# Optimization experiments

Measured on AMD Instinct MI355X. Metric: run time of the kernel, lower is better.

## Reference

```python
import jax, jax.numpy as jnp
import numpy as np

NUM_SLOTS = 8
SLOT_DIM = 256
ITERS = 3
EPS = 1e-8
SCALE = SLOT_DIM ** -0.5


def _ln(x, g, b, eps=1e-5):
    m = jnp.mean(x, axis=-1, keepdims=True)
    v = jnp.mean(jnp.square(x - m), axis=-1, keepdims=True)
    return (x - m) * jax.lax.rsqrt(v + eps) * g + b


def setup_inputs() -> dict:
    key = jax.random.key(0)
    ks = jax.random.split(key, 16)
    b, n, c = 32, 1024, 256
    d = SLOT_DIM
    def xavier(k, shape):
        fan_in, fan_out = shape[1], shape[0]
        lim = np.sqrt(6.0 / (fan_in + fan_out))
        return jax.random.uniform(k, shape, jnp.float32, -lim, lim)
    lim_mu = np.sqrt(6.0 / (1 + d))
    return {
        "inputs": jax.random.normal(ks[0], (b, n, c), jnp.float32),
        "noise": jax.random.normal(ks[1], (b, NUM_SLOTS, d), jnp.float32),
        "slots_mu": jax.random.uniform(ks[2], (1, 1, d), jnp.float32, -lim_mu, lim_mu),
        "slots_log_sigma": jax.random.uniform(ks[3], (1, 1, d), jnp.float32, -lim_mu, lim_mu),
        "Wq": xavier(ks[4], (d, d)),
        "Wk": xavier(ks[5], (d, c)),
        "Wv": xavier(ks[6], (d, c)),
        "gru_wih": xavier(ks[7], (3 * d, d)),
        "gru_whh": xavier(ks[8], (3 * d, d)),
        "gru_bih": jnp.zeros((3 * d,), jnp.float32),
        "gru_bhh": jnp.zeros((3 * d,), jnp.float32),
        "mlp_w1": xavier(ks[9], (4 * d, d)),
        "mlp_b1": jnp.zeros((4 * d,), jnp.float32),
        "mlp_w2": xavier(ks[10], (d, 4 * d)),
        "mlp_b2": jnp.zeros((d,), jnp.float32),
        "ln_in_g": jnp.ones((c,), jnp.float32),
        "ln_in_b": jnp.zeros((c,), jnp.float32),
        "ln_s_g": jnp.ones((d,), jnp.float32),
        "ln_s_b": jnp.zeros((d,), jnp.float32),
        "ln_ff_g": jnp.ones((d,), jnp.float32),
        "ln_ff_b": jnp.zeros((d,), jnp.float32),
    }


def reference(inputs, noise, slots_mu, slots_log_sigma, Wq, Wk, Wv,
              gru_wih, gru_whh, gru_bih, gru_bhh,
              mlp_w1, mlp_b1, mlp_w2, mlp_b2,
              ln_in_g, ln_in_b, ln_s_g, ln_s_b, ln_ff_g, ln_ff_b):
    b = inputs.shape[0]
    d = SLOT_DIM
    # slots ~ N(mu, sigma) reparameterized with given noise
    slots = slots_mu + jnp.exp(slots_log_sigma) * noise  # [b, S, d]
    x = _ln(inputs, ln_in_g, ln_in_b)
    k = jnp.einsum('bnc,dc->bnd', x, Wk)
    v = jnp.einsum('bnc,dc->bnd', x, Wv)
    for _ in range(ITERS):
        slots_prev = slots
        s = _ln(slots, ln_s_g, ln_s_b)
        q = jnp.einsum('bid,ed->bie', s, Wq)
        dots = jnp.einsum('bid,bjd->bij', q, k) * SCALE  # [b, S, n]
        attn = jax.nn.softmax(dots, axis=1) + EPS         # softmax over slots
        attn = attn / jnp.sum(attn, axis=-1, keepdims=True)
        updates = jnp.einsum('bjd,bij->bid', v, attn)      # [b, S, d]
        # GRUCell: x=updates, h=slots_prev (flattened over batch*slots)
        u = updates.reshape(-1, d)
        h = slots_prev.reshape(-1, d)
        gi = u @ gru_wih.T + gru_bih
        gh = h @ gru_whh.T + gru_bhh
        i_r, i_z, i_n = jnp.split(gi, 3, axis=-1)
        h_r, h_z, h_n = jnp.split(gh, 3, axis=-1)
        r = jax.nn.sigmoid(i_r + h_r)
        z = jax.nn.sigmoid(i_z + h_z)
        nn_ = jnp.tanh(i_n + r * h_n)
        slots = ((1.0 - z) * nn_ + z * h).reshape(b, -1, d)
        ff = _ln(slots, ln_ff_g, ln_ff_b)
        ff = jax.nn.relu(ff @ mlp_w1.T + mlp_b1) @ mlp_w2.T + mlp_b2
        slots = slots + ff
    return slots
```

## Files before the change

kernel.cpp:

```cpp
#include <hip/hip_runtime.h>


typedef __attribute__((ext_vector_type(8))) __bf16 bf16x8;
typedef __attribute__((ext_vector_type(4))) float  f32x4;

#define MFMA16(a, b, c) __builtin_amdgcn_mfma_f32_16x16x32_bf16((a), (b), (c), 0, 0, 0)

static __device__ __forceinline__ unsigned short f2bf(float f) {
    unsigned int x = __float_as_uint(f);
    x = (x + 0x7fffu + ((x >> 16) & 1u)) >> 16;
    return (unsigned short)x;
}
static __device__ __forceinline__ float bf2f(unsigned short u) {
    return __uint_as_float((unsigned int)u << 16);
}
static __device__ __forceinline__ float bflo(unsigned int x) {
    return __uint_as_float(x << 16);
}
static __device__ __forceinline__ float bfhi(unsigned int x) {
    return __uint_as_float(x & 0xffff0000u);
}

struct Params {
    const float *inputs, *noise, *mu, *ls;
    const float *Wq, *Wk, *Wv, *wih, *whh, *bih, *bhh, *w1, *b1, *w2, *b2;
    const float *ln_in_g, *ln_in_b, *ln_s_g, *ln_s_b, *ln_ff_g, *ln_ff_b;
    float* out;
    unsigned short *x_bf, *kvW_bf, *Wq_bf, *wih_bf, *whh_bf, *w1_bf, *w2_bf;
    unsigned short *kv_bf, *h_bf, *ff_bf, *h1_bf;
    float *slots, *q, *upart, *rspart, *gi, *gh, *opart;
};

static __device__ void qgemm(const Params& p, const unsigned short (&u)[16][264], int r0) {
    const int t = threadIdx.x, w = t >> 6, lane = t & 63;
    const int lr = lane & 15, lq = lane >> 4;
    f32x4 acc[4] = {};
    for (int k0 = 0; k0 < 256; k0 += 32) {
        bf16x8 a = *(const bf16x8*)&u[lr][k0 + lq * 8];
        #pragma unroll
        for (int j = 0; j < 4; ++j) {
            bf16x8 bv = *(const bf16x8*)(p.Wq_bf + (size_t)(w * 64 + j * 16 + lr) * 256 + k0 + lq * 8);
            acc[j] = MFMA16(a, bv, acc[j]);
        }
    }
    #pragma unroll
    for (int j = 0; j < 4; ++j)
        #pragma unroll
        for (int r = 0; r < 4; ++r)
            p.q[(size_t)(r0 + lq * 4 + r) * 256 + w * 64 + j * 16 + lr] = acc[j][r];
}

__global__ __launch_bounds__(256) void k_prep(Params p) {
    const int bid = blockIdx.x, t = threadIdx.x;
    for (int gid = bid * 256 + t; gid < 1179648; gid += 4608 * 256) {
        if      (gid <   65536) p.kvW_bf[gid]          = f2bf(p.Wk[gid]);
        else if (gid <  131072) p.kvW_bf[gid]          = f2bf(p.Wv[gid -   65536]);
        else if (gid <  196608) p.Wq_bf[gid - 131072]  = f2bf(p.Wq[gid -  131072]);
        else if (gid <  393216) p.wih_bf[gid - 196608] = f2bf(p.wih[gid - 196608]);
        else if (gid <  589824) p.whh_bf[gid - 393216] = f2bf(p.whh[gid - 393216]);
        else if (gid <  851968) p.w1_bf[gid - 589824]  = f2bf(p.w1[gid -  589824]);
        else if (gid < 1114112) p.w2_bf[gid - 851968]  = f2bf(p.w2[gid -  851968]);
        else {
            const int i = gid - 1114112;
            const int d = i & 255;
            p.slots[i] = p.mu[d] + expf(p.ls[d]) * p.noise[i];
        }
    }
    const int wid  = (bid * 256 + t) >> 6;
    const int lane = t & 63;
    const float g0 = p.ln_in_g[lane * 4 + 0], g1 = p.ln_in_g[lane * 4 + 1];
    const float g2 = p.ln_in_g[lane * 4 + 2], g3 = p.ln_in_g[lane * 4 + 3];
    const float b0 = p.ln_in_b[lane * 4 + 0], b1 = p.ln_in_b[lane * 4 + 1];
    const float b2 = p.ln_in_b[lane * 4 + 2], b3 = p.ln_in_b[lane * 4 + 3];
    #pragma unroll 2
    for (int row = wid; row < 32768; row += 18432) {
        float4 v = *(const float4*)(p.inputs + (size_t)row * 256 + lane * 4);
        float s  = v.x + v.y + v.z + v.w;
        float ss = v.x * v.x + v.y * v.y + v.z * v.z + v.w * v.w;
        #pragma unroll
        for (int o = 1; o < 64; o <<= 1) { s += __shfl_xor(s, o); ss += __shfl_xor(ss, o); }
        float mean = s * (1.f / 256.f);
        float var  = ss * (1.f / 256.f) - mean * mean;
        float rstd = rsqrtf(var + 1e-5f);
        ushort4 o4;
        o4.x = f2bf((v.x - mean) * rstd * g0 + b0);
        o4.y = f2bf((v.y - mean) * rstd * g1 + b1);
        o4.z = f2bf((v.z - mean) * rstd * g2 + b2);
        o4.w = f2bf((v.w - mean) * rstd * g3 + b3);
        *(ushort4*)(p.x_bf + (size_t)row * 256 + lane * 4) = o4;
    }
}

union KvSmem {
    struct { unsigned short As[128 * 32], Bs[128 * 32]; } g;
    unsigned short u[16][264];
};

__global__ __launch_bounds__(256) void k_kv(Params p) {
    __shared__ KvSmem sm;
    const int bid = blockIdx.x, t = threadIdx.x;
    if (bid < 1024) {
        const int m0 = (bid >> 2) * 128, n0 = (bid & 3) * 128;
        const int wave = t >> 6, lane = t & 63;
        const int qr = (wave >> 1) * 64, qc = (wave & 1) * 64;
        const int lr = lane & 15, lq = lane >> 4;
        f32x4 acc[4][4] = {};
        const int sr = t >> 2, sl = t & 3, gk = sl * 8;
        const int wsl0 = (sl ^ ((sr >> 1) & 3)) * 8;
        const int wsl1 = (sl ^ (((sr + 64) >> 1) & 3)) * 8;
        for (int k0 = 0; k0 < 256; k0 += 32) {
            __syncthreads();
            uint4 a0 = *(const uint4*)(p.x_bf   + (size_t)(m0 + sr)      * 256 + k0 + gk);
            uint4 a1 = *(const uint4*)(p.x_bf   + (size_t)(m0 + sr + 64) * 256 + k0 + gk);
            uint4 b0 = *(const uint4*)(p.kvW_bf + (size_t)(n0 + sr)      * 256 + k0 + gk);
            uint4 b1 = *(const uint4*)(p.kvW_bf + (size_t)(n0 + sr + 64) * 256 + k0 + gk);
            *(uint4*)(sm.g.As + sr * 32 + wsl0) = a0;
            *(uint4*)(sm.g.As + (sr + 64) * 32 + wsl1) = a1;
            *(uint4*)(sm.g.Bs + sr * 32 + wsl0) = b0;
            *(uint4*)(sm.g.Bs + (sr + 64) * 32 + wsl1) = b1;
            __syncthreads();
            bf16x8 af[4], bv[4];
            #pragma unroll
            for (int i = 0; i < 4; i++) {
                const int ra = qr + i * 16 + lr;
                af[i] = *(const bf16x8*)(sm.g.As + ra * 32 + ((lq ^ ((ra >> 1) & 3)) * 8));
            }
            #pragma unroll
            for (int i = 0; i < 4; i++) {
                const int rb = qc + i * 16 + lr;
                bv[i] = *(const bf16x8*)(sm.g.Bs + rb * 32 + ((lq ^ ((rb >> 1) & 3)) * 8));
            }
            #pragma unroll
            for (int i = 0; i < 4; i++)
                #pragma unroll
                for (int j = 0; j < 4; j++)
                    acc[i][j] = MFMA16(af[i], bv[j], acc[i][j]);
        }
        #pragma unroll
        for (int i = 0; i < 4; i++)
            #pragma unroll
            for (int j = 0; j < 4; j++) {
                const int col = n0 + qc + j * 16 + lr;
                #pragma unroll
                for (int r = 0; r < 4; r++) {
                    const int rw = m0 + qr + i * 16 + lq * 4 + r;
                    p.kv_bf[(size_t)rw * 512 + col] = f2bf(acc[i][j][r]);
                }
            }
    } else {
        const int r0 = (bid - 1024) * 16;
        const int row16 = t >> 4, sub = t & 15;
        float vals[16]; float s = 0.f, ss = 0.f;
        #pragma unroll
        for (int k = 0; k < 16; k += 4) {
            float4 v = *(const float4*)(p.slots + (size_t)(r0 + row16) * 256 + sub * 16 + k);
            vals[k] = v.x; vals[k + 1] = v.y; vals[k + 2] = v.z; vals[k + 3] = v.w;
            s += v.x + v.y + v.z + v.w;
            ss += v.x * v.x + v.y * v.y + v.z * v.z + v.w * v.w;
        }
        #pragma unroll
        for (int m = 1; m < 16; m <<= 1) { s += __shfl_xor(s, m); ss += __shfl_xor(ss, m); }
        const float mean = s * (1.f / 256.f);
        const float var  = ss * (1.f / 256.f) - mean * mean;
        const float rstd = rsqrtf(var + 1e-5f);
        #pragma unroll
        for (int k = 0; k < 16; ++k) {
            const int c = sub * 16 + k;
            p.h_bf[(size_t)(r0 + row16) * 256 + c] = f2bf(vals[k]);
            sm.u[row16][c] = f2bf((vals[k] - mean) * rstd * p.ln_s_g[c] + p.ln_s_b[c]);
        }
        __syncthreads();
        qgemm(p, sm.u, r0);
    }
}

union AtSmem {
    struct { float q[8][260]; float sc[8][132]; } at;
    struct { unsigned short As[64 * 32], Bs[64 * 32]; } g;
};

__global__ __launch_bounds__(256) void k_attn_gh(Params p) {
    __shared__ AtSmem sm;
    const int bid = blockIdx.x, t = threadIdx.x;
    if (bid < 256) {
        const int b = bid >> 3, chunk = bid & 7, j0 = chunk * 128;
        {
            const int i = t >> 5, c0 = (t & 31) * 8;
            const float* qr = p.q + (size_t)(b * 8 + i) * 256 + c0;
            *(float4*)&sm.at.q[i][c0]     = *(const float4*)(qr);
            *(float4*)&sm.at.q[i][c0 + 4] = *(const float4*)(qr + 4);
        }
        __syncthreads();
        {
            const int i = t & 7, jj = t >> 3;
            const float4* qrow = (const float4*)&sm.at.q[i][0];
            #pragma unroll 1
            for (int g = 0; g < 4; ++g) {
                const int jl = g * 32 + jj;
                const uint4* krow = (const uint4*)(p.kv_bf + ((size_t)b * 1024 + j0 + jl) * 512);
                float a0 = 0, a1 = 0, a2 = 0, a3 = 0;
                #pragma unroll 8
                for (int dd = 0; dd < 32; ++dd) {
                    uint4 kk = krow[dd];
                    float4 q0 = qrow[2 * dd], q1 = qrow[2 * dd + 1];
                    a0 += q0.x * bflo(kk.x); a1 += q0.y * bfhi(kk.x);
                    a2 += q0.z * bflo(kk.y); a3 += q0.w * bfhi(kk.y);
                    a0 += q1.x * bflo(kk.z); a1 += q1.y * bfhi(kk.z);
                    a2 += q1.z * bflo(kk.w); a3 += q1.w * bfhi(kk.w);
                }
                sm.at.sc[i][jl] = (a0 + a1 + a2 + a3) * 0.0625f;
            }
        }
        __syncthreads();
        if (t < 128) {
            float v[8], m = -1e30f;
            #pragma unroll
            for (int ii = 0; ii < 8; ++ii) { v[ii] = sm.at.sc[ii][t]; m = fmaxf(m, v[ii]); }
            float s = 0.f;
            #pragma unroll
            for (int ii = 0; ii < 8; ++ii) { v[ii] = __expf(v[ii] - m); s += v[ii]; }
            const float inv = 1.f / s;
            #pragma unroll
            for (int ii = 0; ii < 8; ++ii) sm.at.sc[ii][t] = v[ii] * inv + 1e-8f;
        }
        __syncthreads();
        if (t < 8) {
            float s = 0.f;
            for (int jl = 0; jl < 128; ++jl) s += sm.at.sc[t][jl];
            p.rspart[((size_t)b * 8 + chunk) * 8 + t] = s;
        }
        {
            float acc[8] = {};
            const unsigned short* vbase = p.kv_bf + ((size_t)b * 1024 + j0) * 512 + 256 + t;
            #pragma unroll 8
            for (int jl = 0; jl < 128; ++jl) {
                const float vv = bf2f(vbase[(size_t)jl * 512]);
                #pragma unroll
                for (int ii = 0; ii < 8; ++ii) acc[ii] += sm.at.sc[ii][jl] * vv;
            }
            float* up = p.upart + (((size_t)b * 8 + chunk) * 8) * 256 + t;
            #pragma unroll
            for (int ii = 0; ii < 8; ++ii) up[ii * 256] = acc[ii];
        }
    } else {
        const int g = bid - 256;
        const int m0 = (g & 3) * 64, n0 = (g >> 2) * 64;
        const int wave = t >> 6, lane = t & 63;
        const int lr = lane & 15, lq = lane >> 4;
        f32x4 acc[4] = {};
        const int sr = t >> 2, sl = t & 3, gk = sl * 8;
        const int wsl = (sl ^ ((sr >> 1) & 3)) * 8;
        for (int k0 = 0; k0 < 256; k0 += 32) {
            __syncthreads();
            uint4 a0 = *(const uint4*)(p.h_bf   + (size_t)(m0 + sr) * 256 + k0 + gk);
            uint4 b0 = *(const uint4*)(p.whh_bf + (size_t)(n0 + sr) * 256 + k0 + gk);
            *(uint4*)(sm.g.As + sr * 32 + wsl) = a0;
            *(uint4*)(sm.g.Bs + sr * 32 + wsl) = b0;
            __syncthreads();
            const int ra = wave * 16 + lr;
            bf16x8 af = *(const bf16x8*)(sm.g.As + ra * 32 + ((lq ^ ((ra >> 1) & 3)) * 8));
            #pragma unroll
            for (int j = 0; j < 4; ++j) {
                const int rb = j * 16 + lr;
                bf16x8 bv = *(const bf16x8*)(sm.g.Bs + rb * 32 + ((lq ^ ((rb >> 1) & 3)) * 8));
                acc[j] = MFMA16(af, bv, acc[j]);
            }
        }
        #pragma unroll
        for (int j = 0; j < 4; ++j) {
            const int col = n0 + j * 16 + lr;
            #pragma unroll
            for (int r = 0; r < 4; ++r)
                p.gh[(size_t)(m0 + wave * 16 + lq * 4 + r) * 768 + col] = acc[j][r];
        }
    }
}

__global__ __launch_bounds__(256) void k_gi(Params p) {
    __shared__ unsigned short uS[8][2048];
    __shared__ unsigned short Bs[64 * 32];
    __shared__ float rs_l[64];
    const int t = threadIdx.x;
    const int m0 = blockIdx.x * 64, n0 = blockIdx.y * 64;
    if (t < 64) {
        const int grow = m0 + t, b = grow >> 3, i = grow & 7;
        float rs = 0.f;
        #pragma unroll
        for (int c = 0; c < 8; ++c) rs += p.rspart[((size_t)b * 8 + c) * 8 + i];
        rs_l[t] = 1.f / rs;
    }
    __syncthreads();
    {
        const int sl = (t >> 3) & 3, kc = t >> 5, k7 = t & 7;
        for (int r = 0; r < 64; ++r) {
            const int grow = m0 + r, b = grow >> 3, i = grow & 7;
            float a = 0.f;
            #pragma unroll
            for (int c = 0; c < 8; ++c)
                a += p.upart[(((size_t)b * 8 + c) * 8 + i) * 256 + t];
            uS[kc][r * 32 + ((sl ^ ((r >> 1) & 3)) * 8) + k7] = f2bf(a * rs_l[r]);
        }
    }
    const int wave = t >> 6, lane = t & 63;
    const int lr = lane & 15, lq = lane >> 4;
    f32x4 acc[4] = {};
    const int sr = t >> 2, sl2 = t & 3, gk = sl2 * 8;
    const int wsl = (sl2 ^ ((sr >> 1) & 3)) * 8;
    for (int k0 = 0; k0 < 256; k0 += 32) {
        __syncthreads();
        uint4 b0 = *(const uint4*)(p.wih_bf + (size_t)(n0 + sr) * 256 + k0 + gk);
        *(uint4*)(Bs + sr * 32 + wsl) = b0;
        __syncthreads();
        const int ra = wave * 16 + lr;
        bf16x8 af = *(const bf16x8*)(uS[k0 >> 5] + ra * 32 + ((lq ^ ((ra >> 1) & 3)) * 8));
        #pragma unroll
        for (int j = 0; j < 4; ++j) {
            const int rb = j * 16 + lr;
            bf16x8 bv = *(const bf16x8*)(Bs + rb * 32 + ((lq ^ ((rb >> 1) & 3)) * 8));
            acc[j] = MFMA16(af, bv, acc[j]);
        }
    }
    #pragma unroll
    for (int j = 0; j < 4; ++j) {
        const int col = n0 + j * 16 + lr;
        #pragma unroll
        for (int r = 0; r < 4; ++r)
            p.gi[(size_t)(m0 + wave * 16 + lq * 4 + r) * 768 + col] = acc[j][r];
    }
}

__global__ __launch_bounds__(256) void k_gruln(Params p) {
    __shared__ float red[8];
    const int row = blockIdx.x, t = threadIdx.x;
    const float* gir = p.gi + (size_t)row * 768;
    const float* ghr = p.gh + (size_t)row * 768;
    const float ir  = gir[t]       + p.bih[t];
    const float iz  = gir[256 + t] + p.bih[256 + t];
    const float in_ = gir[512 + t] + p.bih[512 + t];
    const float hr  = ghr[t]       + p.bhh[t];
    const float hz  = ghr[256 + t] + p.bhh[256 + t];
    const float hn  = ghr[512 + t] + p.bhh[512 + t];
    const float r = 1.f / (1.f + __expf(-(ir + hr)));
    const float z = 1.f / (1.f + __expf(-(iz + hz)));
    const float n = tanhf(in_ + r * hn);
    const float h = p.slots[(size_t)row * 256 + t];
    const float s = (1.f - z) * n + z * h;
    p.slots[(size_t)row * 256 + t] = s;
    float sm = s, ssq = s * s;
    #pragma unroll
    for (int o = 32; o > 0; o >>= 1) { sm += __shfl_down(sm, o); ssq += __shfl_down(ssq, o); }
    if ((t & 63) == 0) { red[t >> 6] = sm; red[4 + (t >> 6)] = ssq; }
    __syncthreads();
    const float S  = red[0] + red[1] + red[2] + red[3];
    const float SS = red[4] + red[5] + red[6] + red[7];
    const float mean = S * (1.f / 256.f);
    const float var  = SS * (1.f / 256.f) - mean * mean;
    const float rstd = rsqrtf(var + 1e-5f);
    p.ff_bf[(size_t)row * 256 + t] = f2bf((s - mean) * rstd * p.ln_ff_g[t] + p.ln_ff_b[t]);
}

__global__ __launch_bounds__(256) void k_mlp1(Params p) {
    __shared__ unsigned short As[64 * 32], Bs[64 * 32];
    const int m0 = blockIdx.x * 64, n0 = blockIdx.y * 64;
    const int t = threadIdx.x, wave = t >> 6, lane = t & 63;
    const int lr = lane & 15, lq = lane >> 4;
    f32x4 acc[4] = {};
    const int sr = t >> 2, sl = t & 3, gk = sl * 8;
    const int wsl = (sl ^ ((sr >> 1) & 3)) * 8;
    for (int k0 = 0; k0 < 256; k0 += 32) {
        __syncthreads();
        uint4 a0 = *(const uint4*)(p.ff_bf + (size_t)(m0 + sr) * 256 + k0 + gk);
        uint4 b0 = *(const uint4*)(p.w1_bf + (size_t)(n0 + sr) * 256 + k0 + gk);
        *(uint4*)(As + sr * 32 + wsl) = a0;
        *(uint4*)(Bs + sr * 32 + wsl) = b0;
        __syncthreads();
        const int ra = wave * 16 + lr;
        bf16x8 af = *(const bf16x8*)(As + ra * 32 + ((lq ^ ((ra >> 1) & 3)) * 8));
        #pragma unroll
        for (int j = 0; j < 4; ++j) {
            const int rb = j * 16 + lr;
            bf16x8 bv = *(const bf16x8*)(Bs + rb * 32 + ((lq ^ ((rb >> 1) & 3)) * 8));
            acc[j] = MFMA16(af, bv, acc[j]);
        }
    }
    #pragma unroll
    for (int j = 0; j < 4; ++j) {
        const int col = n0 + j * 16 + lr;
        const float bb = p.b1[col];
        #pragma unroll
        for (int r = 0; r < 4; ++r) {
            const int row = m0 + wave * 16 + lq * 4 + r;
            p.h1_bf[(size_t)row * 1024 + col] = f2bf(fmaxf(acc[j][r] + bb, 0.f));
        }
    }
}

__global__ __launch_bounds__(256) void k_out(Params p) {
    __shared__ unsigned short a_s[16][264];
    const int t = threadIdx.x;
    const int r0 = blockIdx.x * 16, kb = blockIdx.y * 256;
    const int row16 = t >> 4, sub = t & 15;
    {
        const unsigned short* src = p.h1_bf + (size_t)(r0 + row16) * 1024 + kb + sub * 16;
        *(uint4*)&a_s[row16][sub * 16]     = *(const uint4*)(src);
        *(uint4*)&a_s[row16][sub * 16 + 8] = *(const uint4*)(src + 8);
    }
    __syncthreads();
    const int w = t >> 6, lane = t & 63;
    const int lr = lane & 15, lq = lane >> 4;
    f32x4 acc[4] = {};
    for (int k0 = 0; k0 < 256; k0 += 32) {
        bf16x8 a = *(const bf16x8*)&a_s[lr][k0 + lq * 8];
        #pragma unroll
        for (int j = 0; j < 4; ++j) {
            bf16x8 bv = *(const bf16x8*)(p.w2_bf + (size_t)(w * 64 + j * 16 + lr) * 1024 + kb + k0 + lq * 8);
            acc[j] = MFMA16(a, bv, acc[j]);
        }
    }
    #pragma unroll
    for (int j = 0; j < 4; ++j)
        #pragma unroll
        for (int r = 0; r < 4; ++r)
            p.opart[((size_t)blockIdx.y * 256 + r0 + lq * 4 + r) * 256 + w * 64 + j * 16 + lr] = acc[j][r];
}

template<int LAST>
__global__ __launch_bounds__(256) void k_lnq(Params p) {
    __shared__ unsigned short u[16][264];
    const int t = threadIdx.x;
    const int r0 = blockIdx.x * 16;
    const int row16 = t >> 4, sub = t & 15;
    float vals[16]; float s_ = 0.f, ss = 0.f;
    #pragma unroll
    for (int k = 0; k < 16; ++k) {
        const int c = sub * 16 + k;
        const size_t ridx = (size_t)(r0 + row16) * 256 + c;
        float v = p.opart[(size_t)(r0 + row16) * 256 + c]
                + p.opart[((size_t)256 + r0 + row16) * 256 + c]
                + p.opart[((size_t)512 + r0 + row16) * 256 + c]
                + p.opart[((size_t)768 + r0 + row16) * 256 + c]
                + p.b2[c] + p.slots[ridx];
        if (LAST) { p.out[ridx] = v; }
        else {
            p.slots[ridx] = v;
            p.h_bf[ridx]  = f2bf(v);
        }
        vals[k] = v; s_ += v; ss += v * v;
    }
    if (LAST) return;
    #pragma unroll
    for (int m = 1; m < 16; m <<= 1) { s_ += __shfl_xor(s_, m); ss += __shfl_xor(ss, m); }
    const float mean = s_ * (1.f / 256.f);
    const float var  = ss * (1.f / 256.f) - mean * mean;
    const float rstd = rsqrtf(var + 1e-5f);
    #pragma unroll
    for (int k = 0; k < 16; ++k) {
        const int c = sub * 16 + k;
        u[row16][c] = f2bf((vals[k] - mean) * rstd * p.ln_s_g[c] + p.ln_s_b[c]);
    }
    __syncthreads();
    qgemm(p, u, r0);
}

extern "C" void kernel_launch(void* const* d_in, const int* in_sizes, int n_in,
                              void* d_out, int out_size, void* d_ws, size_t ws_size,
                              hipStream_t stream)
{
    (void)in_sizes; (void)n_in; (void)out_size; (void)ws_size;

    Params prm;
    prm.inputs  = (const float*)d_in[0];
    prm.noise   = (const float*)d_in[1];
    prm.mu      = (const float*)d_in[2];
    prm.ls      = (const float*)d_in[3];
    prm.Wq      = (const float*)d_in[4];
    prm.Wk      = (const float*)d_in[5];
    prm.Wv      = (const float*)d_in[6];
    prm.wih     = (const float*)d_in[7];
    prm.whh     = (const float*)d_in[8];
    prm.bih     = (const float*)d_in[9];
    prm.bhh     = (const float*)d_in[10];
    prm.w1      = (const float*)d_in[11];
    prm.b1      = (const float*)d_in[12];
    prm.w2      = (const float*)d_in[13];
    prm.b2      = (const float*)d_in[14];
    prm.ln_in_g = (const float*)d_in[15];
    prm.ln_in_b = (const float*)d_in[16];
    prm.ln_s_g  = (const float*)d_in[17];
    prm.ln_s_b  = (const float*)d_in[18];
    prm.ln_ff_g = (const float*)d_in[19];
    prm.ln_ff_b = (const float*)d_in[20];
    prm.out     = (float*)d_out;

    char* ptr = (char*)d_ws;
    auto alloc = [&](size_t bytes) -> char* {
        char* r = ptr; ptr += (bytes + 255) & ~(size_t)255; return r;
    };
    prm.x_bf   = (unsigned short*)alloc((size_t)32768 * 256 * 2);
    prm.kv_bf  = (unsigned short*)alloc((size_t)32768 * 512 * 2);
    prm.kvW_bf = (unsigned short*)alloc(512 * 256 * 2);
    prm.Wq_bf  = (unsigned short*)alloc(256 * 256 * 2);
    prm.wih_bf = (unsigned short*)alloc(768 * 256 * 2);
    prm.whh_bf = (unsigned short*)alloc(768 * 256 * 2);
    prm.w1_bf  = (unsigned short*)alloc(1024 * 256 * 2);
    prm.w2_bf  = (unsigned short*)alloc(256 * 1024 * 2);
    prm.slots  = (float*)         alloc(256 * 256 * 4);
    prm.q      = (float*)         alloc(256 * 256 * 4);
    prm.upart  = (float*)         alloc((size_t)32 * 8 * 8 * 256 * 4);
    prm.rspart = (float*)         alloc(32 * 8 * 8 * 4);
    prm.h_bf   = (unsigned short*)alloc(256 * 256 * 2);
    prm.gi     = (float*)         alloc(256 * 768 * 4);
    prm.gh     = (float*)         alloc(256 * 768 * 4);
    prm.ff_bf  = (unsigned short*)alloc(256 * 256 * 2);
    prm.h1_bf  = (unsigned short*)alloc(256 * 1024 * 2);
    prm.opart  = (float*)         alloc((size_t)4 * 256 * 256 * 4);

    k_prep<<<4608, 256, 0, stream>>>(prm);
    k_kv  <<<1040, 256, 0, stream>>>(prm);
    for (int it = 0; it < 3; ++it) {
        k_attn_gh<<<304, 256, 0, stream>>>(prm);
        k_gi     <<<dim3(4, 12), 256, 0, stream>>>(prm);
        k_gruln  <<<256, 256, 0, stream>>>(prm);
        k_mlp1   <<<dim3(4, 16), 256, 0, stream>>>(prm);
        k_out    <<<dim3(16, 4), 256, 0, stream>>>(prm);
        if (it < 2) k_lnq<0><<<16, 256, 0, stream>>>(prm);
        else        k_lnq<1><<<16, 256, 0, stream>>>(prm);
    }
}
```

Before: 356.9 us.

## Split attention over finer token chunks and add separate u reduction kernel

The attention stage now splits each batch into 16 token chunks of 64 instead of 8 of 128, doubling the block count to better fill the GPU's compute units. The per-slot partial reduction and normalization, previously done redundantly inside every k_gi block (each of 12 column blocks re-reduced upart), moves into a new small k_u2b kernel that writes a bf16 u matrix once. k_gi then becomes a plain tiled GEMM loading A from global memory. The cost is an extra kernel launch per iteration and twice as many partial buffers to write and reduce.

```diff
diff --git a/kernel.cpp b/kernel.cpp
--- a/kernel.cpp
+++ b/kernel.cpp
@@ -27,7 +27,7 @@
     const float *ln_in_g, *ln_in_b, *ln_s_g, *ln_s_b, *ln_ff_g, *ln_ff_b;
     float* out;
     unsigned short *x_bf, *kvW_bf, *Wq_bf, *wih_bf, *whh_bf, *w1_bf, *w2_bf;
-    unsigned short *kv_bf, *h_bf, *ff_bf, *h1_bf;
+    unsigned short *kv_bf, *u_bf, *h_bf, *ff_bf, *h1_bf;
     float *slots, *q, *upart, *rspart, *gi, *gh, *opart;
 };
 
@@ -175,15 +175,15 @@
 }
 
 union AtSmem {
-    struct { float q[8][260]; float sc[8][132]; } at;
+    struct { float q[8][260]; float sc[8][68]; } at;
     struct { unsigned short As[64 * 32], Bs[64 * 32]; } g;
 };
 
 __global__ __launch_bounds__(256) void k_attn_gh(Params p) {
     __shared__ AtSmem sm;
     const int bid = blockIdx.x, t = threadIdx.x;
-    if (bid < 256) {
-        const int b = bid >> 3, chunk = bid & 7, j0 = chunk * 128;
+    if (bid < 512) {
+        const int b = bid >> 4, chunk = bid & 15, j0 = chunk * 64;
         {
             const int i = t >> 5, c0 = (t & 31) * 8;
             const float* qr = p.q + (size_t)(b * 8 + i) * 256 + c0;
@@ -195,7 +195,7 @@
             const int i = t & 7, jj = t >> 3;
             const float4* qrow = (const float4*)&sm.at.q[i][0];
             #pragma unroll 1
-            for (int g = 0; g < 4; ++g) {
+            for (int g = 0; g < 2; ++g) {
                 const int jl = g * 32 + jj;
                 const uint4* krow = (const uint4*)(p.kv_bf + ((size_t)b * 1024 + j0 + jl) * 512);
                 float a0 = 0, a1 = 0, a2 = 0, a3 = 0;
@@ -212,7 +212,7 @@
             }
         }
         __syncthreads();
-        if (t < 128) {
+        if (t < 64) {
             float v[8], m = -1e30f;
             #pragma unroll
             for (int ii = 0; ii < 8; ++ii) { v[ii] = sm.at.sc[ii][t]; m = fmaxf(m, v[ii]); }
@@ -226,24 +226,24 @@
         __syncthreads();
         if (t < 8) {
             float s = 0.f;
-            for (int jl = 0; jl < 128; ++jl) s += sm.at.sc[t][jl];
-            p.rspart[((size_t)b * 8 + chunk) * 8 + t] = s;
+            for (int jl = 0; jl < 64; ++jl) s += sm.at.sc[t][jl];
+            p.rspart[((size_t)b * 16 + chunk) * 8 + t] = s;
         }
         {
             float acc[8] = {};
             const unsigned short* vbase = p.kv_bf + ((size_t)b * 1024 + j0) * 512 + 256 + t;
             #pragma unroll 8
-            for (int jl = 0; jl < 128; ++jl) {
+            for (int jl = 0; jl < 64; ++jl) {
                 const float vv = bf2f(vbase[(size_t)jl * 512]);
                 #pragma unroll
                 for (int ii = 0; ii < 8; ++ii) acc[ii] += sm.at.sc[ii][jl] * vv;
             }
-            float* up = p.upart + (((size_t)b * 8 + chunk) * 8) * 256 + t;
+            float* up = p.upart + (((size_t)b * 16 + chunk) * 8) * 256 + t;
             #pragma unroll
             for (int ii = 0; ii < 8; ++ii) up[ii * 256] = acc[ii];
         }
     } else {
-        const int g = bid - 256;
+        const int g = bid - 512;
         const int m0 = (g & 3) * 64, n0 = (g >> 2) * 64;
         const int wave = t >> 6, lane = t & 63;
         const int lr = lane & 15, lq = lane >> 4;
@@ -276,43 +276,35 @@
     }
 }
 
+__global__ __launch_bounds__(256) void k_u2b(Params p) {
+    const int row = blockIdx.x, t = threadIdx.x;
+    const int b = row >> 3, i = row & 7;
+    float acc = 0.f, rs = 0.f;
+    #pragma unroll
+    for (int c = 0; c < 16; ++c) {
+        acc += p.upart[(((size_t)b * 16 + c) * 8 + i) * 256 + t];
+        rs  += p.rspart[((size_t)b * 16 + c) * 8 + i];
+    }
+    p.u_bf[(size_t)row * 256 + t] = f2bf(acc / rs);
+}
+
 __global__ __launch_bounds__(256) void k_gi(Params p) {
-    __shared__ unsigned short uS[8][2048];
-    __shared__ unsigned short Bs[64 * 32];
-    __shared__ float rs_l[64];
-    const int t = threadIdx.x;
+    __shared__ unsigned short As[64 * 32], Bs[64 * 32];
     const int m0 = blockIdx.x * 64, n0 = blockIdx.y * 64;
-    if (t < 64) {
-        const int grow = m0 + t, b = grow >> 3, i = grow & 7;
-        float rs = 0.f;
-        #pragma unroll
-        for (int c = 0; c < 8; ++c) rs += p.rspart[((size_t)b * 8 + c) * 8 + i];
-        rs_l[t] = 1.f / rs;
-    }
-    __syncthreads();
-    {
-        const int sl = (t >> 3) & 3, kc = t >> 5, k7 = t & 7;
-        for (int r = 0; r < 64; ++r) {
-            const int grow = m0 + r, b = grow >> 3, i = grow & 7;
-            float a = 0.f;
-            #pragma unroll
-            for (int c = 0; c < 8; ++c)
-                a += p.upart[(((size_t)b * 8 + c) * 8 + i) * 256 + t];
-            uS[kc][r * 32 + ((sl ^ ((r >> 1) & 3)) * 8) + k7] = f2bf(a * rs_l[r]);
-        }
-    }
-    const int wave = t >> 6, lane = t & 63;
+    const int t = threadIdx.x, wave = t >> 6, lane = t & 63;
     const int lr = lane & 15, lq = lane >> 4;
     f32x4 acc[4] = {};
-    const int sr = t >> 2, sl2 = t & 3, gk = sl2 * 8;
-    const int wsl = (sl2 ^ ((sr >> 1) & 3)) * 8;
+    const int sr = t >> 2, sl = t & 3, gk = sl * 8;
+    const int wsl = (sl ^ ((sr >> 1) & 3)) * 8;
     for (int k0 = 0; k0 < 256; k0 += 32) {
         __syncthreads();
+        uint4 a0 = *(const uint4*)(p.u_bf   + (size_t)(m0 + sr) * 256 + k0 + gk);
         uint4 b0 = *(const uint4*)(p.wih_bf + (size_t)(n0 + sr) * 256 + k0 + gk);
+        *(uint4*)(As + sr * 32 + wsl) = a0;
         *(uint4*)(Bs + sr * 32 + wsl) = b0;
         __syncthreads();
         const int ra = wave * 16 + lr;
-        bf16x8 af = *(const bf16x8*)(uS[k0 >> 5] + ra * 32 + ((lq ^ ((ra >> 1) & 3)) * 8));
+        bf16x8 af = *(const bf16x8*)(As + ra * 32 + ((lq ^ ((ra >> 1) & 3)) * 8));
         #pragma unroll
         for (int j = 0; j < 4; ++j) {
             const int rb = j * 16 + lr;
@@ -506,8 +498,9 @@
     prm.w2_bf  = (unsigned short*)alloc(256 * 1024 * 2);
     prm.slots  = (float*)         alloc(256 * 256 * 4);
     prm.q      = (float*)         alloc(256 * 256 * 4);
-    prm.upart  = (float*)         alloc((size_t)32 * 8 * 8 * 256 * 4);
-    prm.rspart = (float*)         alloc(32 * 8 * 8 * 4);
+    prm.upart  = (float*)         alloc((size_t)32 * 16 * 8 * 256 * 4);
+    prm.rspart = (float*)         alloc(32 * 16 * 8 * 4);
+    prm.u_bf   = (unsigned short*)alloc(256 * 256 * 2);
     prm.h_bf   = (unsigned short*)alloc(256 * 256 * 2);
     prm.gi     = (float*)         alloc(256 * 768 * 4);
     prm.gh     = (float*)         alloc(256 * 768 * 4);
@@ -518,7 +511,8 @@
     k_prep<<<4608, 256, 0, stream>>>(prm);
     k_kv  <<<1040, 256, 0, stream>>>(prm);
     for (int it = 0; it < 3; ++it) {
-        k_attn_gh<<<304, 256, 0, stream>>>(prm);
+        k_attn_gh<<<560, 256, 0, stream>>>(prm);
+        k_u2b    <<<256, 256, 0, stream>>>(prm);
         k_gi     <<<dim3(4, 12), 256, 0, stream>>>(prm);
         k_gruln  <<<256, 256, 0, stream>>>(prm);
         k_mlp1   <<<dim3(4, 16), 256, 0, stream>>>(prm);
```

Result: faster. 296.2 us (-17.0%).
